# Performance work log

Hardware: AMD Instinct MI355X
Metric: run time of the kernel (lower is better)

The kernel has to match this reference:

```python
import jax, jax.numpy as jnp
import numpy as np

N, B, PG, L, HC, EC, H, NC, KNN = 256, 4, 64, 32, 128, 64, 4, 14, 8
D = HC // H
CUTOFF = 10.0
LOG2 = 0.6931471805599453

_counts = np.array([14, 5, 11, 8, 8, 6, 9, 9, 4, 10, 8, 8, 9, 8, 11, 7, 6, 7, 14, 12, 7])
RES_ATOM_MASK = (np.arange(14)[None, :] < _counts[:, None]).astype(np.float32)  # [21,14]


def _ln(x, g, b):
    mu = jnp.mean(x, -1, keepdims=True)
    var = jnp.mean((x - mu) ** 2, -1, keepdims=True)
    return (x - mu) / jnp.sqrt(var + 1e-5) * g + b


def _ssp(x):
    return jax.nn.softplus(x) - LOG2


def _safe_norm(x):
    return jnp.sqrt(jnp.maximum(jnp.sum(x * x, -1), 1e-12))


def _seg_softmax(x, idx, n):
    m = jax.ops.segment_max(x, idx, num_segments=n)
    e = jnp.exp(x - m[idx])
    s = jax.ops.segment_sum(e, idx, num_segments=n)
    return e / s[idx]


def _smear(d):
    offs = jnp.linspace(0.0, CUTOFF, EC)
    coeff = -0.5 / (offs[1] - offs[0]) ** 2
    return jnp.exp(coeff * (d[..., None] - offs) ** 2)


def _core(res_H, res_X, ligand_pos, ligand_feat, ligand_mask,
          ln_g, ln_b, ln1_g, ln1_b,
          WQ, WK, WV, WKl, WVl, WO, WOl, WOl1,
          Ti_w1, Ti_b1, Ti_w2, Ti_b2,
          sD_w1, sD_b1, sD_w2, sD_b2,
          sD1_w1, sD1_b1, sD1_w2, sD1_b2,
          res_S, batch, residue_mask, row1, col1):
    n = res_H.shape[0]
    bsz = ligand_feat.shape[0]
    lc = ligand_feat.shape[1]
    amask = jnp.asarray(RES_ATOM_MASK)[res_S]  # [n,14]

    # kNN graph on C-alpha (atom 1), per-graph, flow target_to_source, + self loops
    ctr = res_X[:, 1]
    d2 = jnp.sum((ctr[:, None] - ctr[None]) ** 2, -1)
    bad = (batch[:, None] != batch[None]) | jnp.eye(n, dtype=bool)
    _, nbr = jax.lax.top_k(-jnp.where(bad, jnp.inf, d2), KNN)
    row = jnp.concatenate([jnp.repeat(jnp.arange(n), KNN), jnp.arange(n)])
    col = jnp.concatenate([nbr.reshape(-1), jnp.arange(n)])

    Rij = _safe_norm(res_X[row][:, :, None] - res_X[col][:, None])  # [E,14,14]
    drep = _smear(Rij)  # [E,14,14,EC]

    res_Hn = _ln(res_H, ln_g, ln_b)
    Q = (res_Hn @ WQ.T).reshape(n, NC, H, D)
    Kt = (res_Hn @ WK.T).reshape(n, NC, H, D)
    V = (res_Hn @ WV.T).reshape(n, NC, H, D)

    logits = jnp.einsum('ephd,eqhd->ehpq', Q[row], Kt[col]) / np.sqrt(D)
    sig = jax.nn.relu(drep @ sD_w1.T + sD_b1) @ sD_w2.T + sD_b2  # [E,14,14,H]
    logits = logits + sig.transpose(0, 3, 1, 2)

    am_e = amask[row][:, :, None] * amask[col][:, None]  # [E,14,14]
    r = jnp.einsum('ep,ehpq,eq->eh', amask[row], logits, amask[col])
    r = r / jnp.sum(am_e, (-1, -2))[:, None]
    beta = _seg_softmax(r, row, n)  # [E,H]

    att = jax.nn.softmax(logits, -1) * am_e[:, None]
    att = att / (jnp.sum(jnp.abs(att), -1, keepdims=True) + 1e-7)
    aV = jnp.einsum('ehpq,eqhd->ehpd', att, V[col])
    updH = jax.ops.segment_sum(beta[:, :, None, None] * aV, row, num_segments=n)
    updH = updH.transpose(0, 2, 1, 3).reshape(n, NC, HC)
    res_H2 = (res_Hn + _ssp(updH) @ WO.T) * amask[..., None]

    Xij = res_X[row][:, :, None] - res_X[col][:, None]  # [E,14,14,3]
    Xij = Xij / (_safe_norm(Xij)[..., None] + 1e-5)
    Qf = Q.reshape(n, NC, HC)
    Kf = Kt.reshape(n, NC, HC)
    # T_i on concat([Q_p, K_q, dist]) computed as split matmuls (no big concat)
    hmid = (Qf[row] @ Ti_w1[:, :HC].T)[:, :, None, :] \
        + (Kf[col] @ Ti_w1[:, HC:2 * HC].T)[:, None, :, :] \
        + drep @ Ti_w1[:, 2 * HC:].T + Ti_b1  # [E,14,14,HC]
    f = (jax.nn.relu(hmid) @ Ti_w2.T + Ti_b2)[..., 0]  # [E,14,14]
    f = f * jnp.mean(att, 1)
    dX = jax.ops.segment_sum(jnp.mean(beta, -1)[:, None, None]
                             * jnp.sum(f[..., None] * Xij, -2), row, num_segments=n)
    res_X2 = jnp.where(residue_mask[:, None, None],
                       res_X + jnp.clip(dX, -3.0, 3.0), res_X)

    # residue <-> ligand cross attention over (editable residue, graph) edges
    lf = _ln(ligand_feat, ln1_g, ln1_b)
    Kl = (lf @ WKl.T).reshape(bsz, lc, H, D)
    Vl = (lf @ WVl.T).reshape(bsz, lc, H, D)
    Rij1 = _safe_norm(res_X2[row1][:, :, None] - ligand_pos[col1][:, None])
    drep1 = _smear(Rij1)  # [E1,14,L,EC]
    lg = jnp.einsum('ephd,eqhd->ehpq', Q[row1], Kl[col1]) / np.sqrt(D)
    sig1 = jax.nn.relu(drep1 @ sD1_w1.T + sD1_b1) @ sD1_w2.T + sD1_b2
    lg = lg + sig1.transpose(0, 3, 1, 2)

    am1 = amask[row1][:, :, None] * ligand_mask[col1][:, None]  # [E1,14,L]
    r1 = jnp.einsum('ep,ehpq,eq->eh', amask[row1], lg, ligand_mask[col1])
    r1 = r1 / jnp.sum(am1, (-1, -2))[:, None]
    beta1 = _seg_softmax(r1, col1, bsz)

    ar = jax.nn.softmax(lg, -1) * am1[:, None]
    ar = ar / (jnp.sum(jnp.abs(ar), -1, keepdims=True) + 1e-7)
    al = jax.nn.softmax(lg, -2) * am1[:, None]
    # faithful to source: lig branch divided by L1 norm of already-normalized ar
    al = al / (jnp.sum(jnp.abs(ar), -1, keepdims=True) + 1e-7)
    aVr = jnp.einsum('ehpq,eqhd->ehpd', ar, Vl[col1])  # [E1,H,14,D]
    e1 = row1.shape[0]
    res_H3 = res_H2.at[row1].add(
        _ssp(aVr.transpose(0, 2, 1, 3).reshape(e1, NC, HC)) @ WOl.T)
    res_H3 = res_H3 * amask[..., None]
    aVlg = jnp.einsum('ehpq,ephd->ehqd', al, V[row1])  # [E1,H,L,D]
    updL = jax.ops.segment_sum(beta1[:, :, None, None] * aVlg, col1, num_segments=bsz)
    lf2 = lf + _ssp(updL.transpose(0, 2, 1, 3).reshape(bsz, lc, HC)) @ WOl1.T
    return res_H3, res_X2, lf2


def setup_inputs() -> dict:
    key = jax.random.key(0)
    ks = jax.random.split(key, 40)
    rn = lambda i, shape, s=1.0: jax.random.normal(ks[i], shape, jnp.float32) * s
    w = lambda i, shape: jax.random.normal(ks[i], shape, jnp.float32) * 0.05
    res_H = rn(0, (N, NC, HC))
    res_X = rn(1, (N, NC, 3), 4.0)
    res_S = jax.random.randint(ks[2], (N,), 0, 21)
    batch = jnp.repeat(jnp.arange(B), PG)
    residue_mask = (jnp.arange(N) % PG) < 16
    row1 = jnp.asarray(np.nonzero(np.asarray(residue_mask))[0])
    col1 = row1 // PG
    ligand_pos = rn(3, (B, L, 3), 4.0)
    ligand_feat = rn(4, (B, L, HC))
    ligand_mask = jnp.tile((jnp.arange(L) < 24).astype(jnp.float32)[None], (B, 1))
    return dict(
        res_H=res_H, res_X=res_X, ligand_pos=ligand_pos, ligand_feat=ligand_feat,
        ligand_mask=ligand_mask,
        ln_g=jnp.ones((HC,)), ln_b=jnp.zeros((HC,)),
        ln1_g=jnp.ones((HC,)), ln1_b=jnp.zeros((HC,)),
        WQ=w(5, (HC, HC)), WK=w(6, (HC, HC)), WV=w(7, (HC, HC)),
        WKl=w(8, (HC, HC)), WVl=w(9, (HC, HC)),
        WO=w(10, (HC, HC)), WOl=w(11, (HC, HC)), WOl1=w(12, (HC, HC)),
        Ti_w1=w(13, (HC, 2 * HC + EC)), Ti_b1=jnp.zeros((HC,)),
        Ti_w2=w(14, (1, HC)), Ti_b2=jnp.zeros((1,)),
        sD_w1=w(15, (HC, EC)), sD_b1=jnp.zeros((HC,)),
        sD_w2=w(16, (H, HC)), sD_b2=jnp.zeros((H,)),
        sD1_w1=w(17, (HC, EC)), sD1_b1=jnp.zeros((HC,)),
        sD1_w2=w(18, (H, HC)), sD1_b2=jnp.zeros((H,)),
        res_S=res_S, batch=batch, residue_mask=residue_mask, row1=row1, col1=col1)


def reference(res_H, res_X, ligand_pos, ligand_feat, ligand_mask,
              ln_g, ln_b, ln1_g, ln1_b,
              WQ, WK, WV, WKl, WVl, WO, WOl, WOl1,
              Ti_w1, Ti_b1, Ti_w2, Ti_b2,
              sD_w1, sD_b1, sD_w2, sD_b2,
              sD1_w1, sD1_b1, sD1_w2, sD1_b2,
              res_S, batch, residue_mask, row1, col1):
    return _core(res_H, res_X, ligand_pos, ligand_feat, ligand_mask,
                 ln_g, ln_b, ln1_g, ln1_b,
                 WQ, WK, WV, WKl, WVl, WO, WOl, WOl1,
                 Ti_w1, Ti_b1, Ti_w2, Ti_b2,
                 sD_w1, sD_b1, sD_w2, sD_b2,
                 sD1_w1, sD1_b1, sD1_w2, sD1_b2,
                 res_S, batch, residue_mask, row1, col1)
```

## Files before the change

kernel.cpp:

```cpp
#include <hip/hip_runtime.h>
#include <hip/hip_bf16.h>
#include <math.h>

typedef __hip_bfloat16 bf16;

#define NRES 256
#define LC   32
#define HCH  128
#define ECH  64
#define NH   4
#define NCA  14
#define KNNK 8
#define DH   32
#define NKE  (NRES*KNNK)
#define NEDGE (NKE+NRES)
#define NE1  64
#define NROWS (NRES*NCA)

#define NT     3073
#define TSCALE 256.0f
#define DMAXT  12.0f

#define O_RESH   0
#define O_RESX   458752
#define O_LPOS   469504
#define O_LFEAT  469888
#define O_LMASK  486272
#define O_LNG    486400
#define O_LNB    486528
#define O_LN1G   486656
#define O_LN1B   486784
#define O_WQ     486912
#define O_WK     503296
#define O_WV     519680
#define O_WKL    536064
#define O_WVL    552448
#define O_WO     568832
#define O_WOL    585216
#define O_WOL1   601600
#define O_TIW1   617984
#define O_TIB1   658944
#define O_TIW2   659072
#define O_TIB2   659200
#define O_SDW1   659204
#define O_SDB1   667396
#define O_SDW2   667524
#define O_SDB2   668036
#define O_SD1W1  668040
#define O_SD1B1  676232
#define O_SD1W2  676360
#define O_SD1B2  676872
#define TOTCVT   676876
#define CVT_RSV  676880

#define OUTX_OFF 458752
#define OUTL_OFF 469504

__constant__ int c_counts[21] = {14,5,11,8,8,6,9,9,4,10,8,8,9,8,11,7,6,7,14,12,7};

__device__ __forceinline__ float b2f(bf16 x){ return __bfloat162float(x); }
__device__ __forceinline__ float sspf(float x){
  return fmaxf(x,0.f) + log1pf(expf(-fabsf(x))) - 0.6931471805599453f;
}
__device__ __forceinline__ float bflo(unsigned u){ return __uint_as_float(u<<16); }
__device__ __forceinline__ float bfhi(unsigned u){ return __uint_as_float(u & 0xffff0000u); }
__device__ __forceinline__ unsigned short f2bs(float v){ bf16 b=__float2bfloat16(v); return *(unsigned short*)&b; }
__device__ __forceinline__ unsigned pack2(float a, float b){
  return (unsigned)f2bs(a) | ((unsigned)f2bs(b)<<16);
}
__device__ __forceinline__ int ccount(int s){ return c_counts[s<0?0:(s>20?20:s)]; }
__device__ __forceinline__ void storeOut(void* out, int isbf, int idx, float v){
  if (isbf) ((bf16*)out)[idx] = __float2bfloat16(v);
  else      ((float*)out)[idx] = v;
}

__global__ __launch_bounds__(256) void kcvt(
    const void* s0,const void* s1,const void* s2,const void* s3,const void* s4,
    const void* s5,const void* s6,const void* s7,const void* s8,const void* s9,
    const void* s10,const void* s11,const void* s12,const void* s13,const void* s14,
    const void* s15,const void* s16,const void* s17,const void* s18,const void* s19,
    const void* s20,const void* s21,const void* s22,const void* s23,const void* s24,
    const void* s25,const void* s26,const void* s27,const void* s28,
    float* __restrict__ dst, int* __restrict__ flag)
{
  __shared__ int sflag;
  int tid = threadIdx.x;
  if (tid < 64){
    unsigned w = ((const unsigned*)s0)[tid];
    unsigned lo = w & 0xFFFFu;
    int ee = (lo >> 7) & 0xFF;
    int good = (lo == 0u) || (ee >= 121 && ee <= 133);
    unsigned long long m = __ballot(good);
    if (tid == 0){
      sflag = (__popcll(m) >= 40) ? 1 : 0;
      if (blockIdx.x == 0) flag[0] = sflag;
    }
  }
  __syncthreads();
  int isbf = sflag;
  int g = blockIdx.x*256 + tid;
  if (g >= TOTCVT) return;
  const void* src; int l;
  if      (g < O_RESX ) { src=s0;  l=g; }
  else if (g < O_LPOS ) { src=s1;  l=g-O_RESX; }
  else if (g < O_LFEAT) { src=s2;  l=g-O_LPOS; }
  else if (g < O_LMASK) { src=s3;  l=g-O_LFEAT; }
  else if (g < O_LNG  ) { src=s4;  l=g-O_LMASK; }
  else if (g < O_LNB  ) { src=s5;  l=g-O_LNG; }
  else if (g < O_LN1G ) { src=s6;  l=g-O_LNB; }
  else if (g < O_LN1B ) { src=s7;  l=g-O_LN1G; }
  else if (g < O_WQ   ) { src=s8;  l=g-O_LN1B; }
  else if (g < O_WK   ) { src=s9;  l=g-O_WQ; }
  else if (g < O_WV   ) { src=s10; l=g-O_WK; }
  else if (g < O_WKL  ) { src=s11; l=g-O_WV; }
  else if (g < O_WVL  ) { src=s12; l=g-O_WKL; }
  else if (g < O_WO   ) { src=s13; l=g-O_WVL; }
  else if (g < O_WOL  ) { src=s14; l=g-O_WO; }
  else if (g < O_WOL1 ) { src=s15; l=g-O_WOL; }
  else if (g < O_TIW1 ) { src=s16; l=g-O_WOL1; }
  else if (g < O_TIB1 ) { src=s17; l=g-O_TIW1; }
  else if (g < O_TIW2 ) { src=s18; l=g-O_TIB1; }
  else if (g < O_TIB2 ) { src=s19; l=g-O_TIW2; }
  else if (g < O_SDW1 ) { src=s20; l=0; }
  else if (g < O_SDB1 ) { src=s21; l=g-O_SDW1; }
  else if (g < O_SDW2 ) { src=s22; l=g-O_SDB1; }
  else if (g < O_SDB2 ) { src=s23; l=g-O_SDW2; }
  else if (g < O_SD1W1) { src=s24; l=g-O_SDB2; }
  else if (g < O_SD1B1) { src=s25; l=g-O_SD1W1; }
  else if (g < O_SD1W2) { src=s26; l=g-O_SD1B1; }
  else if (g < O_SD1B2) { src=s27; l=g-O_SD1W2; }
  else                  { src=s28; l=g-O_SD1B2; }
  float v = isbf ? b2f(((const bf16*)src)[l]) : ((const float*)src)[l];
  dst[g] = v;
}

__global__ __launch_bounds__(128) void kprep(const float* __restrict__ cvt, const int* __restrict__ row1,
    float* __restrict__ cT, float* __restrict__ sigT, float* __restrict__ sig1T,
    float* __restrict__ wt, int* __restrict__ inv_row)
{
  int b = blockIdx.x, o = threadIdx.x;
  if (b >= NT){
    int cb = b - NT;
    if (cb < 1280){
      int gid = cb*128 + o;
      int m = gid >> 14;
      int j = gid & 16383;
      int oo = j >> 7, c = j & 127;
      float v;
      switch(m){
        case 0: v = cvt[O_WQ  + j]; break;
        case 1: v = cvt[O_WK  + j]; break;
        case 2: v = cvt[O_WV  + j]; break;
        case 3: v = cvt[O_WO  + j]; break;
        case 4: v = cvt[O_WKL + j]; break;
        case 5: v = cvt[O_WVL + j]; break;
        case 6: v = cvt[O_WOL + j]; break;
        case 7: v = cvt[O_WOL1+ j]; break;
        case 8: v = cvt[O_TIW1 + oo*320 + c]; break;
        default:v = cvt[O_TIW1 + oo*320 + 128 + c]; break;
      }
      wt[m*16384 + c*128 + oo] = v;
    } else {
      for (int i=o;i<NRES;i+=128) inv_row[i] = -1;
      __syncthreads();
      if (o < NE1) inv_row[row1[o] & 255] = o;
    }
    return;
  }
  __shared__ float dr[64];
  __shared__ float W[128*65];
  __shared__ float h1[128], h1b[128];
  float d = (float)b * (1.0f/256.0f);
  const float step = 10.0f/63.0f;
  const float coef = -0.5f/(step*step);
  if (o < 64){ float t = d - step*(float)o; dr[o] = expf(coef*t*t); }
  for (int idx=o; idx<8192; idx+=128){ int oo=idx>>6, k=idx&63; W[oo*65+k] = cvt[O_TIW1 + oo*320 + 256 + k]; }
  __syncthreads();
  {
    float c = cvt[O_TIB1+o];
    for (int k=0;k<64;k++) c += dr[k]*W[o*65+k];
    cT[b*128+o] = c;
  }
  __syncthreads();
  for (int idx=o; idx<8192; idx+=128){ int oo=idx>>6, k=idx&63; W[oo*65+k] = cvt[O_SDW1 + idx]; }
  __syncthreads();
  {
    float a = cvt[O_SDB1+o];
    for (int k=0;k<64;k++) a += dr[k]*W[o*65+k];
    h1[o] = fmaxf(a,0.f);
  }
  __syncthreads();
  for (int idx=o; idx<8192; idx+=128){ int oo=idx>>6, k=idx&63; W[oo*65+k] = cvt[O_SD1W1 + idx]; }
  __syncthreads();
  {
    float a2 = cvt[O_SD1B1+o];
    for (int k=0;k<64;k++) a2 += dr[k]*W[o*65+k];
    h1b[o] = fmaxf(a2,0.f);
  }
  __syncthreads();
  if (o < 8){
    int h = o & 3;
    const float* hh = (o<4)? h1 : h1b;
    int wbase = (o<4)? O_SDW2 : O_SD1W2;
    int bbase = (o<4)? O_SDB2 : O_SD1B2;
    float s = cvt[bbase + h];
    for (int k=0;k<128;k++) s += hh[k]*cvt[wbase + h*128 + k];
    if (o<4) sigT[b*4+h] = s; else sig1T[b*4+h] = s;
  }
}

__global__ __launch_bounds__(256) void kProjAll(
    const float* __restrict__ cvt, const float* __restrict__ wt, const int* __restrict__ batch,
    float* __restrict__ resHn, bf16* __restrict__ Qw16, bf16* __restrict__ Kw16,
    bf16* __restrict__ Vw16, bf16* __restrict__ TQw16, bf16* __restrict__ TKw16,
    int* __restrict__ nbr, float* __restrict__ lf, bf16* __restrict__ Klw16, bf16* __restrict__ Vlw16)
{
  __shared__ float Xs[16*129];
  __shared__ float x2[2][HCH];
  __shared__ float sred2[2][2];
  int bb = blockIdx.x, tid = threadIdx.x;

  if (bb < 672){
    int m = bb / 224;
    int rt = (bb % 224) * 16;
    for (int i=tid; i<16*128; i+=256){
      int r=i>>7, c=i&127;
      Xs[r*129+c] = cvt[O_RESH + (rt+r)*HCH + c];
    }
    __syncthreads();
    {
      int wave = tid>>6, lane = tid&63;
      int r = wave*4 + (lane>>4);
      int cb = lane & 15;
      float s=0;
      #pragma unroll
      for (int j=0;j<8;j++) s += Xs[r*129 + cb + 16*j];
      #pragma unroll
      for (int off=1; off<16; off<<=1) s += __shfl_xor(s, off);
      float mu = s*(1.f/HCH);
      float q=0;
      #pragma unroll
      for (int j=0;j<8;j++){ float dv = Xs[r*129+cb+16*j]-mu; q += dv*dv; }
      #pragma unroll
      for (int off=1; off<16; off<<=1) q += __shfl_xor(q, off);
      float inv = rsqrtf(q*(1.f/HCH) + 1e-5f);
      #pragma unroll
      for (int j=0;j<8;j++){
        int c = cb + 16*j;
        float xh = (Xs[r*129+c]-mu)*inv*cvt[O_LNG+c] + cvt[O_LNB+c];
        Xs[r*129+c] = xh;
        if (m==0) resHn[(rt+r)*HCH+c] = xh;
      }
    }
    __syncthreads();
    int tc = (tid & 31) * 4;
    int tr = (tid >> 5) * 2;
    const float* W = wt + m*16384;
    float a00=0,a01=0,a02=0,a03=0, a10=0,a11=0,a12=0,a13=0;
    for (int c=0;c<HCH;c++){
      float4 w4 = *(const float4*)(W + c*128 + tc);
      float x0 = Xs[tr*129 + c];
      float x1 = Xs[(tr+1)*129 + c];
      a00 += x0*w4.x; a01 += x0*w4.y; a02 += x0*w4.z; a03 += x0*w4.w;
      a10 += x1*w4.x; a11 += x1*w4.y; a12 += x1*w4.z; a13 += x1*w4.w;
    }
    bf16* out = (m==0)? Qw16 : (m==1)? Kw16 : Vw16;
    {
      unsigned* o0 = (unsigned*)(out + (rt+tr  )*HCH + tc);
      unsigned* o1 = (unsigned*)(out + (rt+tr+1)*HCH + tc);
      o0[0]=pack2(a00,a01); o0[1]=pack2(a02,a03);
      o1[0]=pack2(a10,a11); o1[1]=pack2(a12,a13);
    }
    if (m == 2) return;
    __syncthreads();
    Xs[tr*129+tc]=a00; Xs[tr*129+tc+1]=a01; Xs[tr*129+tc+2]=a02; Xs[tr*129+tc+3]=a03;
    Xs[(tr+1)*129+tc]=a10; Xs[(tr+1)*129+tc+1]=a11; Xs[(tr+1)*129+tc+2]=a12; Xs[(tr+1)*129+tc+3]=a13;
    __syncthreads();
    const float* W2 = wt + (8+m)*16384;
    a00=0;a01=0;a02=0;a03=0; a10=0;a11=0;a12=0;a13=0;
    for (int c=0;c<HCH;c++){
      float4 w4 = *(const float4*)(W2 + c*128 + tc);
      float x0 = Xs[tr*129 + c];
      float x1 = Xs[(tr+1)*129 + c];
      a00 += x0*w4.x; a01 += x0*w4.y; a02 += x0*w4.z; a03 += x0*w4.w;
      a10 += x1*w4.x; a11 += x1*w4.y; a12 += x1*w4.z; a13 += x1*w4.w;
    }
    bf16* out2 = m ? TKw16 : TQw16;
    {
      unsigned* o0 = (unsigned*)(out2 + (rt+tr  )*HCH + tc);
      unsigned* o1 = (unsigned*)(out2 + (rt+tr+1)*HCH + tc);
      o0[0]=pack2(a00,a01); o0[1]=pack2(a02,a03);
      o1[0]=pack2(a10,a11); o1[1]=pack2(a12,a13);
    }
    return;
  }

  if (bb < 736){
    int wave = tid>>6, lane = tid&63;
    int n = (bb-672)*4 + wave;
    float cx = cvt[O_RESX+(n*NCA+1)*3+0];
    float cy = cvt[O_RESX+(n*NCA+1)*3+1];
    float cz = cvt[O_RESX+(n*NCA+1)*3+2];
    int bn = batch[n];
    float d2v[4]; int idv[4];
    #pragma unroll
    for (int t=0;t<4;t++){
      int j = lane + 64*t;
      float jx = cvt[O_RESX+(j*NCA+1)*3+0];
      float jy = cvt[O_RESX+(j*NCA+1)*3+1];
      float jz = cvt[O_RESX+(j*NCA+1)*3+2];
      float dx=cx-jx, dy=cy-jy, dz=cz-jz;
      float d2 = dx*dx+dy*dy+dz*dz;
      bool bad = (batch[j]!=bn) || (j==n);
      d2v[t] = bad ? INFINITY : d2;
      idv[t] = j;
    }
    for (int k=0;k<KNNK;k++){
      float dm = d2v[0]; int im = idv[0];
      #pragma unroll
      for (int t=1;t<4;t++)
        if (d2v[t]<dm || (d2v[t]==dm && idv[t]<im)){ dm=d2v[t]; im=idv[t]; }
      #pragma unroll
      for (int off=1; off<64; off<<=1){
        float dn = __shfl_xor(dm, off);
        int   in = __shfl_xor(im, off);
        if (dn<dm || (dn==dm && in<im)){ dm=dn; im=in; }
      }
      if (lane==0) nbr[n*KNNK+k] = im;
      #pragma unroll
      for (int t=0;t<4;t++) if (idv[t]==im) d2v[t] = INFINITY;
    }
    return;
  }

  int row = tid>>7, t = tid&127;
  int rb = (bb-736)*2 + row;
  float v = cvt[O_LFEAT + rb*HCH + t];
  float s=v;
  for (int off=1; off<64; off<<=1) s += __shfl_xor(s, off);
  if ((t&63)==0) sred2[row][t>>6]=s;
  __syncthreads();
  float mu=(sred2[row][0]+sred2[row][1])*(1.f/HCH);
  __syncthreads();
  float d=v-mu; s=d*d;
  for (int off=1; off<64; off<<=1) s += __shfl_xor(s, off);
  if ((t&63)==0) sred2[row][t>>6]=s;
  __syncthreads();
  float var=(sred2[row][0]+sred2[row][1])*(1.f/HCH);
  float xh = d*rsqrtf(var+1e-5f)*cvt[O_LN1G+t] + cvt[O_LN1B+t];
  x2[row][t]=xh; lf[rb*HCH+t]=xh;
  __syncthreads();
  const float* WKlt = wt + 4*16384;
  const float* WVlt = wt + 5*16384;
  float aK=0.f, aV=0.f;
  for (int c=0;c<HCH;c++){
    float xc=x2[row][c];
    aK += xc*WKlt[c*128+t];
    aV += xc*WVlt[c*128+t];
  }
  Klw16[rb*HCH+t]=__float2bfloat16(aK);
  Vlw16[rb*HCH+t]=__float2bfloat16(aV);
}

__global__ __launch_bounds__(256) void k3_edge(
    const float* __restrict__ cvt, const int* __restrict__ res_S, const int* __restrict__ nbr,
    const bf16* __restrict__ Qw16, const bf16* __restrict__ Kw16,
    const bf16* __restrict__ TQw16, const bf16* __restrict__ TKw16,
    const bf16* __restrict__ Vw16, const float* __restrict__ cT, const float* __restrict__ sigT,
    float* __restrict__ r_ws, bf16* __restrict__ aVe16, float* __restrict__ dXe)
{
  __shared__ unsigned Bq[14*66], Bk[14*66], Tq[14*66], Tk[14*66];
  __shared__ float LG[784], FR[196];
  __shared__ float tw2s[128], tb2s[1], Xr[42], Xc[42], amr[14], amc[14], rpart[56], cnts[2];
  unsigned* Vc = Tq;

  int b = blockIdx.x, tid = threadIdx.x;
  int rr = b & 255, slot = b >> 8;
  int e  = (slot < 8) ? (rr*8 + slot) : (2048 + rr);
  int cc = (slot < 8) ? (nbr[rr*8 + slot] & 255) : rr;

  const unsigned* Q32  = (const unsigned*)Qw16;
  const unsigned* K32  = (const unsigned*)Kw16;
  const unsigned* TQ32 = (const unsigned*)TQw16;
  const unsigned* TK32 = (const unsigned*)TKw16;
  const unsigned* V32  = (const unsigned*)Vw16;

  for (int i=tid;i<NCA*64;i+=256){
    int p=i>>6, k=i&63;
    Bq[p*66+k]=Q32[rr*896+i];  Bk[p*66+k]=K32[cc*896+i];
    Tq[p*66+k]=TQ32[rr*896+i]; Tk[p*66+k]=TK32[cc*896+i];
  }
  if (tid < 128) tw2s[tid]=cvt[O_TIW2+tid];
  if (tid == 128) tb2s[0]=cvt[O_TIB2];
  if (tid >= 136 && tid < 178){
    int i=tid-136; int p=i/3, jx=i%3;
    Xr[i] = cvt[O_RESX+(rr*NCA+p)*3+jx];
    Xc[i] = cvt[O_RESX+(cc*NCA+p)*3+jx];
  }
  if (tid >= 242 && tid < 242+NCA){
    int p=tid-242;
    amr[p] = (p < ccount(res_S[rr])) ? 1.f : 0.f;
    amc[p] = (p < ccount(res_S[cc])) ? 1.f : 0.f;
  }
  __syncthreads();

  if (tid < 196){
    int p = tid/14, q = tid%14;
    float dx=Xr[p*3]-Xc[q*3], dy=Xr[p*3+1]-Xc[q*3+1], dz=Xr[p*3+2]-Xc[q*3+2];
    float d = sqrtf(fmaxf(dx*dx+dy*dy+dz*dz, 1e-12f));
    int i0 = (int)(fminf(d, DMAXT)*TSCALE + 0.5f);
    float4 sg = ((const float4*)sigT)[i0];
    const float4* crow = (const float4*)(cT + i0*128);
    const uint2* Tq2 = (const uint2*)Tq;
    const uint2* Tk2 = (const uint2*)Tk;
    const uint2* Bq2 = (const uint2*)Bq;
    const uint2* Bk2 = (const uint2*)Bk;
    float fa = tb2s[0];
    #pragma unroll 8
    for (int j=0;j<32;j++){
      float4 cb = crow[j];
      uint2 ta = Tq2[p*33 + j];
      uint2 ka = Tk2[q*33 + j];
      int o = 4*j;
      fa += fmaxf(bflo(ta.x)+bflo(ka.x)+cb.x, 0.f)*tw2s[o  ];
      fa += fmaxf(bfhi(ta.x)+bfhi(ka.x)+cb.y, 0.f)*tw2s[o+1];
      fa += fmaxf(bflo(ta.y)+bflo(ka.y)+cb.z, 0.f)*tw2s[o+2];
      fa += fmaxf(bfhi(ta.y)+bfhi(ka.y)+cb.w, 0.f)*tw2s[o+3];
    }
    float qk0=0,qk1=0,qk2=0,qk3=0;
    #pragma unroll
    for (int j=0;j<8;j++){
      uint2 a0=Bq2[p*33+j],    b0=Bk2[q*33+j];
      uint2 a1=Bq2[p*33+8+j],  b1=Bk2[q*33+8+j];
      uint2 a2=Bq2[p*33+16+j], b2=Bk2[q*33+16+j];
      uint2 a3=Bq2[p*33+24+j], b3=Bk2[q*33+24+j];
      qk0 += bflo(a0.x)*bflo(b0.x) + bfhi(a0.x)*bfhi(b0.x) + bflo(a0.y)*bflo(b0.y) + bfhi(a0.y)*bfhi(b0.y);
      qk1 += bflo(a1.x)*bflo(b1.x) + bfhi(a1.x)*bfhi(b1.x) + bflo(a1.y)*bflo(b1.y) + bfhi(a1.y)*bfhi(b1.y);
      qk2 += bflo(a2.x)*bflo(b2.x) + bfhi(a2.x)*bfhi(b2.x) + bflo(a2.y)*bflo(b2.y) + bfhi(a2.y)*bfhi(b2.y);
      qk3 += bflo(a3.x)*bflo(b3.x) + bfhi(a3.x)*bfhi(b3.x) + bflo(a3.y)*bflo(b3.y) + bfhi(a3.y)*bfhi(b3.y);
    }
    const float isq = 0.17677669529663687f;
    LG[0*196+tid] = qk0*isq + sg.x;
    LG[1*196+tid] = qk1*isq + sg.y;
    LG[2*196+tid] = qk2*isq + sg.z;
    LG[3*196+tid] = qk3*isq + sg.w;
    FR[tid] = fa;
  }
  __syncthreads();

  for (int i=tid;i<NCA*64;i+=256){
    int p=i>>6, k=i&63;
    Vc[p*66+k]=V32[cc*896+i];
  }
  if (tid < 56){
    int h=tid/14, pp=tid%14;
    float ap = amr[pp];
    float row[NCA];
    float s=0;
    #pragma unroll
    for (int qq=0;qq<NCA;qq++){ row[qq]=LG[h*196+pp*14+qq]; s += row[qq]*amc[qq]; }
    rpart[h*14+pp] = s*ap;
    float m=-INFINITY;
    #pragma unroll
    for (int qq=0;qq<NCA;qq++) m=fmaxf(m,row[qq]);
    float sum=0;
    #pragma unroll
    for (int qq=0;qq<NCA;qq++){ row[qq]=expf(row[qq]-m); sum+=row[qq]; }
    float inv=1.f/sum, s2=0;
    #pragma unroll
    for (int qq=0;qq<NCA;qq++){ row[qq]=row[qq]*inv*ap*amc[qq]; s2+=row[qq]; }
    float inv2=1.f/(s2+1e-7f);
    #pragma unroll
    for (int qq=0;qq<NCA;qq++) LG[h*196+pp*14+qq]=row[qq]*inv2;
  }
  if (tid == 56){
    float sr=0, sc=0;
    for (int i=0;i<NCA;i++){ sr+=amr[i]; sc+=amc[i]; }
    cnts[0]=sr; cnts[1]=sc;
  }
  __syncthreads();
  if (tid < NH){
    float s=0;
    for (int pp=0;pp<NCA;pp++) s += rpart[tid*14+pp];
    r_ws[e*NH+tid] = s/(cnts[0]*cnts[1]);
  }
  if (tid < 196){
    int p=tid/14, q=tid%14;
    float ma = 0.25f*(LG[p*14+q] + LG[196+p*14+q] + LG[392+p*14+q] + LG[588+p*14+q]);
    FR[tid] *= ma;
  }
  __syncthreads();
  if (tid < NCA){
    int pp=tid;
    float ax=0, ay=0, az=0;
    #pragma unroll
    for (int qq=0;qq<NCA;qq++){
      float dx=Xr[pp*3]-Xc[qq*3], dy=Xr[pp*3+1]-Xc[qq*3+1], dz=Xr[pp*3+2]-Xc[qq*3+2];
      float nrm = sqrtf(fmaxf(dx*dx+dy*dy+dz*dz,1e-12f));
      float sc = FR[pp*14+qq]/(nrm+1e-5f);
      ax += sc*dx; ay += sc*dy; az += sc*dz;
    }
    dXe[(e*NCA+pp)*3+0]=ax; dXe[(e*NCA+pp)*3+1]=ay; dXe[(e*NCA+pp)*3+2]=az;
  }
  unsigned* aVe32 = (unsigned*)aVe16;
  #pragma unroll
  for (int rep=0;rep<4;rep++){
    int jdx = rep*256 + tid;
    if (jdx < 896){
      int h = jdx/224, rem = jdx%224;
      int pp = rem>>4, ddp = rem&15;
      float a0=0, a1=0;
      #pragma unroll
      for (int qq=0;qq<NCA;qq++){
        unsigned v = Vc[qq*66 + h*16 + ddp];
        float l = LG[h*196+pp*14+qq];
        a0 += l*bflo(v);
        a1 += l*bfhi(v);
      }
      aVe32[e*896 + jdx] = pack2(a0,a1);
    }
  }
}

__global__ __launch_bounds__(256) void k4_agg(
    const float* __restrict__ cvt, const int* __restrict__ res_S, const int* __restrict__ inv_row,
    const float* __restrict__ r_ws, const bf16* __restrict__ aVe16, const float* __restrict__ dXe,
    const float* __restrict__ resHn, const float* __restrict__ wt, const int* __restrict__ flag,
    float* __restrict__ resH2, float* __restrict__ resX2, void* __restrict__ d_out)
{
  int n = blockIdx.x, tid = threadIdx.x;
  __shared__ float beta[9][NH];
  __shared__ float betam[9];
  __shared__ float Xs[NCA][HCH];
  if (tid < NH){
    int h = tid;
    float rv[9], m=-INFINITY;
    #pragma unroll
    for (int k=0;k<9;k++){
      int ek = (k<KNNK)? n*KNNK+k : NKE+n;
      rv[k] = r_ws[ek*NH+h];
      m = fmaxf(m, rv[k]);
    }
    float s=0;
    #pragma unroll
    for (int k=0;k<9;k++){ rv[k]=expf(rv[k]-m); s+=rv[k]; }
    #pragma unroll
    for (int k=0;k<9;k++) beta[k][h]=rv[k]/s;
  }
  __syncthreads();
  if (tid < 9) betam[tid] = 0.25f*(beta[tid][0]+beta[tid][1]+beta[tid][2]+beta[tid][3]);
  int col = tid & 127, ph = tid >> 7;
  int h = col>>5, dd = col&31;
  float bh[9];
  #pragma unroll
  for (int k=0;k<9;k++) bh[k]=beta[k][h];
  #pragma unroll
  for (int i=0;i<7;i++){
    int p = ph + 2*i;
    float u=0;
    #pragma unroll
    for (int k=0;k<9;k++){
      int ek = (k<KNNK)? n*KNNK+k : NKE+n;
      u += bh[k]*b2f(aVe16[ek*1792 + h*448 + p*32 + dd]);
    }
    Xs[p][col] = sspf(u);
  }
  __syncthreads();
  const float* WOt = wt + 3*16384;
  float acc[7];
  #pragma unroll
  for (int i=0;i<7;i++) acc[i]=0.f;
  for (int c=0;c<HCH;c++){
    float w = WOt[c*128+col];
    #pragma unroll
    for (int i=0;i<7;i++) acc[i] += Xs[ph+2*i][c]*w;
  }
  int cnt = ccount(res_S[n]);
  #pragma unroll
  for (int i=0;i<7;i++){
    int p = ph + 2*i;
    float am = (p<cnt)?1.f:0.f;
    float outv = (resHn[(n*NCA+p)*HCH+col] + acc[i])*am;
    resH2[(n*NCA+p)*HCH+col] = outv;
  }
  if (tid < NCA*3){
    int isbf = *flag;
    int p=tid/3, jx=tid%3;
    float s=0;
    #pragma unroll
    for (int k=0;k<9;k++){
      int ek=(k<KNNK)? n*KNNK+k : NKE+n;
      s += betam[k]*dXe[(ek*NCA+p)*3+jx];
    }
    float base = cvt[O_RESX+(n*NCA+p)*3+jx];
    float v = (inv_row[n]>=0) ? base + fminf(fmaxf(s,-3.f),3.f) : base;
    resX2[(n*NCA+p)*3+jx] = v;
    storeOut(d_out, isbf, OUTX_OFF + (n*NCA+p)*3+jx, v);
  }
}

__global__ __launch_bounds__(256) void k6_lig(
    const float* __restrict__ cvt, const int* __restrict__ res_S,
    const int* __restrict__ row1, const int* __restrict__ col1,
    const float* __restrict__ resX2, const bf16* __restrict__ Qw16, const bf16* __restrict__ Klw16,
    const bf16* __restrict__ Vw16, const bf16* __restrict__ Vlw16, const float* __restrict__ sig1T,
    float* __restrict__ r1_ws, float* __restrict__ aVr, float* __restrict__ aVlg)
{
  __shared__ __align__(16) float S[10042];
  float* Bq  = S;
  float* Bk  = S + 1848;
  float* LG  = S;
  float* Vl  = S + 1848;
  float* ALs = S + 6104;
  float* Vr  = S + 7896;
  float* EX  = S + 9744;
  float* Xr = EX;
  float* Lp = EX + 42;
  float* amr = EX + 138;
  float* lm  = EX + 152;
  float* s2r = EX + 184;
  float* rpart = EX + 240;
  float* cnts  = EX + 296;
  int e = blockIdx.x, tid = threadIdx.x;
  int rr = row1[e] & 255, cb = col1[e] & 3;

  for (int i=tid;i<NCA*HCH;i+=256){ int p=i>>7,c=i&127; Bq[p*132+c]=b2f(Qw16[rr*1792+i]); Vr[p*132+c]=b2f(Vw16[rr*1792+i]); }
  for (int i=tid;i<LC*HCH;i+=256){ int q=i>>7,c=i&127; Bk[q*133+c]=b2f(Klw16[cb*LC*HCH+i]); }
  if (tid >= 8 && tid < 50){ int i=tid-8; int p=i/3,jx=i%3; Xr[i]=resX2[(rr*NCA+p)*3+jx]; }
  if (tid >= 64 && tid < 160){ int i=tid-64; int q=i/3,jx=i%3; Lp[i]=cvt[O_LPOS+(cb*LC+q)*3+jx]; }
  if (tid >= 160 && tid < 160+NCA) amr[tid-160]=((tid-160) < ccount(res_S[rr]))?1.f:0.f;
  if (tid >= 192 && tid < 224) lm[tid-192]=cvt[O_LMASK + cb*LC + tid-192];
  __syncthreads();

  float l0[2][4];
  int npair = (tid < 192) ? 2 : 1;
  for (int w=0; w<npair; w++){
    int pair = tid + w*256;
    int p = pair>>5, q = pair&31;
    float dx=Xr[p*3]-Lp[q*3], dy=Xr[p*3+1]-Lp[q*3+1], dz=Xr[p*3+2]-Lp[q*3+2];
    float d = sqrtf(fmaxf(dx*dx+dy*dy+dz*dz,1e-12f));
    int i0 = (int)(fminf(d, DMAXT)*TSCALE + 0.5f);
    float4 sg = ((const float4*)sig1T)[i0];
    float q0=0,q1=0,q2=0,q3=0;
    #pragma unroll
    for (int dd=0;dd<DH;dd++){
      q0 += Bq[p*132+dd]   *Bk[q*133+dd];
      q1 += Bq[p*132+32+dd]*Bk[q*133+32+dd];
      q2 += Bq[p*132+64+dd]*Bk[q*133+64+dd];
      q3 += Bq[p*132+96+dd]*Bk[q*133+96+dd];
    }
    const float isq=0.17677669529663687f;
    l0[w][0]=q0*isq+sg.x; l0[w][1]=q1*isq+sg.y; l0[w][2]=q2*isq+sg.z; l0[w][3]=q3*isq+sg.w;
  }
  __syncthreads();
  for (int w=0; w<npair; w++){
    int pair = tid + w*256;
    LG[0*448+pair]=l0[w][0]; LG[1*448+pair]=l0[w][1]; LG[2*448+pair]=l0[w][2]; LG[3*448+pair]=l0[w][3];
  }
  for (int i=tid;i<LC*HCH;i+=256){ int q=i>>7,c=i&127; Vl[q*132+c]=b2f(Vlw16[cb*LC*HCH+i]); }
  __syncthreads();

  if (tid < 56){
    int h=tid/14, pp=tid%14;
    float ap=amr[pp];
    float s=0, m=-INFINITY;
    for (int qq=0;qq<LC;qq++){ float v=LG[h*448+pp*32+qq]; s+=v*lm[qq]; m=fmaxf(m,v); }
    rpart[h*14+pp]=s*ap;
    float sum=0;
    for (int qq=0;qq<LC;qq++) sum+=expf(LG[h*448+pp*32+qq]-m);
    float inv=1.f/sum, s2=0;
    for (int qq=0;qq<LC;qq++) s2 += expf(LG[h*448+pp*32+qq]-m)*inv*ap*lm[qq];
    s2r[h*14+pp] = s2/(s2+1e-7f);
  }
  if (tid==56){
    float sr=0,sl=0;
    for(int i=0;i<NCA;i++) sr+=amr[i];
    for(int i=0;i<LC;i++) sl+=lm[i];
    cnts[0]=sr; cnts[1]=sl;
  }
  __syncthreads();
  if (tid < NH){
    float s=0; for (int pp=0;pp<NCA;pp++) s+=rpart[tid*14+pp];
    r1_ws[e*NH+tid]=s/(cnts[0]*cnts[1]);
  }
  if (tid < NH*LC){
    int h=tid>>5, qq=tid&31;
    float m=-INFINITY;
    for (int pp=0;pp<NCA;pp++) m=fmaxf(m,LG[h*448+pp*32+qq]);
    float sum=0;
    for (int pp=0;pp<NCA;pp++) sum+=expf(LG[h*448+pp*32+qq]-m);
    float inv=1.f/sum;
    float lq=lm[qq];
    for (int pp=0;pp<NCA;pp++){
      float a=expf(LG[h*448+pp*32+qq]-m)*inv*amr[pp]*lq;
      ALs[h*448+pp*32+qq]=a/(s2r[h*14+pp]+1e-7f);
    }
  }
  __syncthreads();
  if (tid < 56){
    int h=tid/14, pp=tid%14;
    float ap=amr[pp];
    float m=-INFINITY;
    for (int qq=0;qq<LC;qq++) m=fmaxf(m,LG[h*448+pp*32+qq]);
    float row[LC];
    float sum=0;
    for (int qq=0;qq<LC;qq++){ row[qq]=expf(LG[h*448+pp*32+qq]-m); sum+=row[qq]; }
    float inv=1.f/sum, s2=0;
    for (int qq=0;qq<LC;qq++){ row[qq]=row[qq]*inv*ap*lm[qq]; s2+=row[qq]; }
    float inv2=1.f/(s2+1e-7f);
    for (int qq=0;qq<LC;qq++) LG[h*448+pp*32+qq]=row[qq]*inv2;
  }
  __syncthreads();
  for (int j=tid;j<NH*NCA*DH;j+=256){
    int h=j/448, rem=j%448, pp=rem>>5, dd=rem&31;
    float acc=0;
    #pragma unroll
    for (int qq=0;qq<LC;qq++) acc += LG[h*448+pp*32+qq]*Vl[qq*132+h*32+dd];
    aVr[e*1792+j]=acc;
  }
  for (int j=tid;j<NH*LC*DH;j+=256){
    int h=j>>10, rem=j&1023, qq=rem>>5, dd=rem&31;
    float acc=0;
    #pragma unroll
    for (int pp=0;pp<NCA;pp++) acc += ALs[h*448+pp*32+qq]*Vr[pp*132+h*32+dd];
    aVlg[e*4096+j]=acc;
  }
}

__global__ __launch_bounds__(256) void k78_final(
    const int* __restrict__ inv_row, const int* __restrict__ res_S, const int* __restrict__ col1,
    const float* __restrict__ resH2, const float* __restrict__ aVr,
    const float* __restrict__ r1_ws, const float* __restrict__ aVlg, const float* __restrict__ lf,
    const float* __restrict__ wt, const int* __restrict__ flag, void* __restrict__ d_out)
{
  int bb = blockIdx.x, tid = threadIdx.x;
  if (bb < 256){
    int n = bb;
    int e = inv_row[n];
    __shared__ float G[NCA][HCH];
    if (e>=0){
      for (int j=tid;j<NCA*HCH;j+=256){
        int h=j/448, rem=j%448, pp=rem>>5, dd=rem&31;
        G[pp][h*DH+dd] = sspf(aVr[e*1792+j]);
      }
    }
    __syncthreads();
    int col = tid & 127, ph = tid >> 7;
    float acc[7];
    #pragma unroll
    for (int i=0;i<7;i++) acc[i]=0.f;
    if (e>=0){
      const float* WOlt = wt + 6*16384;
      for (int c=0;c<HCH;c++){
        float w=WOlt[c*128+col];
        #pragma unroll
        for (int i=0;i<7;i++) acc[i]+=G[ph+2*i][c]*w;
      }
    }
    int cnt=ccount(res_S[n]);
    int isbf = *flag;
    #pragma unroll
    for (int i=0;i<7;i++){
      int p = ph + 2*i;
      float am=(p<cnt)?1.f:0.f;
      float v=(resH2[(n*NCA+p)*HCH+col]+acc[i])*am;
      storeOut(d_out, isbf, (n*NCA+p)*HCH+col, v);
    }
    return;
  }
  int rb = bb - 256;
  int b = rb>>5, q = rb&31;
  __shared__ float bw[NE1][NH];
  __shared__ float xs[HCH];
  if (tid<NH){
    int h=tid;
    float m=-INFINITY;
    for (int e=0;e<NE1;e++) if ((col1[e]&3)==b) m=fmaxf(m, r1_ws[e*NH+h]);
    float s=0;
    for (int e=0;e<NE1;e++) if ((col1[e]&3)==b) s+=expf(r1_ws[e*NH+h]-m);
    for (int e=0;e<NE1;e++) bw[e][h] = ((col1[e]&3)==b)? expf(r1_ws[e*NH+h]-m)/s : 0.f;
  }
  __syncthreads();
  if (tid < 128){
    int h=tid>>5, dd=tid&31;
    float u=0;
    for (int e=0;e<NE1;e++) u += bw[e][h]*aVlg[e*4096 + h*1024 + q*32 + dd];
    xs[tid]=sspf(u);
  }
  __syncthreads();
  if (tid < 128){
    const float* WOl1t = wt + 7*16384;
    float acc=0;
    for (int c=0;c<HCH;c++) acc += xs[c]*WOl1t[c*128+tid];
    float v = lf[rb*HCH+tid] + acc;
    storeOut(d_out, *flag, OUTL_OFF + rb*HCH+tid, v);
  }
}

extern "C" void kernel_launch(void* const* d_in, const int* in_sizes, int n_in,
                              void* d_out, int out_size, void* d_ws, size_t ws_size,
                              hipStream_t stream)
{
  const int* res_S = (const int*)d_in[29];
  const int* batch = (const int*)d_in[30];
  const int* row1  = (const int*)d_in[32];
  const int* col1  = (const int*)d_in[33];

  float* wsf = (float*)d_ws;
  size_t o = 0;
  int*   flag    = (int*)(wsf + o); o += 4;
  float* cvt     = wsf + o; o += CVT_RSV;
  float* wt      = wsf + o; o += 10*16384;
  int*   inv_row = (int*)(wsf + o); o += 256;
  int*   nbr     = (int*)(wsf + o); o += NRES*KNNK;
  float* resHn   = wsf + o; o += NROWS*HCH;
  bf16*  Qw16    = (bf16*)(wsf + o); o += NROWS*HCH/2;
  bf16*  Kw16    = (bf16*)(wsf + o); o += NROWS*HCH/2;
  bf16*  Vw16    = (bf16*)(wsf + o); o += NROWS*HCH/2;
  bf16*  TQw16   = (bf16*)(wsf + o); o += NROWS*HCH/2;
  bf16*  TKw16   = (bf16*)(wsf + o); o += NROWS*HCH/2;
  float* r_ws    = wsf + o; o += NEDGE*NH;
  bf16*  aVe16   = (bf16*)(wsf + o); o += (size_t)NEDGE*1792/2;
  float* dXe     = wsf + o; o += NEDGE*NCA*3;
  float* resH2   = wsf + o; o += NROWS*HCH;
  float* resX2   = wsf + o; o += NRES*NCA*3;
  float* lf      = wsf + o; o += 4*LC*HCH;
  bf16*  Klw16   = (bf16*)(wsf + o); o += 4*LC*HCH/2;
  bf16*  Vlw16   = (bf16*)(wsf + o); o += 4*LC*HCH/2;
  float* r1w     = wsf + o; o += NE1*NH;
  float* aVrw    = wsf + o; o += NE1*1792;
  float* aVlgw   = wsf + o; o += NE1*4096;
  float* cT      = wsf + o; o += (size_t)NT*128;
  float* sigT    = wsf + o; o += NT*4;
  float* sig1T   = wsf + o; o += NT*4;

  kcvt<<<(TOTCVT+255)/256, 256, 0, stream>>>(
      d_in[0],d_in[1],d_in[2],d_in[3],d_in[4],d_in[5],d_in[6],d_in[7],d_in[8],
      d_in[9],d_in[10],d_in[11],d_in[12],d_in[13],d_in[14],d_in[15],d_in[16],
      d_in[17],d_in[18],d_in[19],d_in[20],d_in[21],d_in[22],d_in[23],d_in[24],
      d_in[25],d_in[26],d_in[27],d_in[28], cvt, flag);
  kprep<<<NT + 1280 + 1, 128, 0, stream>>>(cvt, row1, cT, sigT, sig1T, wt, inv_row);
  kProjAll<<<800, 256, 0, stream>>>(cvt, wt, batch, resHn, Qw16, Kw16, Vw16, TQw16, TKw16,
                                    nbr, lf, Klw16, Vlw16);
  k3_edge<<<NEDGE, 256, 0, stream>>>(cvt, res_S, nbr, Qw16, Kw16, TQw16, TKw16, Vw16, cT, sigT,
                                     r_ws, aVe16, dXe);
  k4_agg<<<NRES, 256, 0, stream>>>(cvt, res_S, inv_row, r_ws, aVe16, dXe, resHn, wt, flag,
                                   resH2, resX2, d_out);
  k6_lig<<<NE1, 256, 0, stream>>>(cvt, res_S, row1, col1, resX2, Qw16, Klw16, Vw16, Vlw16, sig1T,
                                  r1w, aVrw, aVlgw);
  k78_final<<<384, 256, 0, stream>>>(inv_row, res_S, col1, resH2, aVrw, r1w, aVlgw, lf,
                                     wt, flag, d_out);
}
```

Measured before the change: 282.6 us.

## Use MFMA bf16 instructions for per-edge QK logits and attention-V products

Replaces the scalar bf16 dot products for the 14x14 per-head QK logits and the attention-weighted V aggregation in the edge kernel with 16x16x32 bf16 MFMA instructions, using XOR-swizzled shared-memory layouts for Q, K and a transposed V. The pairwise trigger-MLP inputs are pre-expanded to fp32 in shared memory so the inner loop no longer unpacks bf16. The aim is to cut ALU work in the edge kernel. In exchange it pads 14 to 16, rounds attention weights to bf16 before the V product, adds an extra barrier, and writes aVe as scattered 2-byte stores.

Result: no change. 285.3 us (+1.0%).

```diff
diff --git a/kernel.cpp b/kernel.cpp
--- a/kernel.cpp
+++ b/kernel.cpp
@@ -57,6 +57,9 @@
 #define OUTL_OFF 469504
 
 __constant__ int c_counts[21] = {14,5,11,8,8,6,9,9,4,10,8,8,9,8,11,7,6,7,14,12,7};
+
+using bfrag = __attribute__((ext_vector_type(8))) short;
+using f32x4 = __attribute__((ext_vector_type(4))) float;
 
 __device__ __forceinline__ float b2f(bf16 x){ return __bfloat162float(x); }
 __device__ __forceinline__ float sspf(float x){
@@ -369,26 +372,53 @@
     const bf16* __restrict__ Vw16, const float* __restrict__ cT, const float* __restrict__ sigT,
     float* __restrict__ r_ws, bf16* __restrict__ aVe16, float* __restrict__ dXe)
 {
-  __shared__ unsigned Bq[14*66], Bk[14*66], Tq[14*66], Tk[14*66];
-  __shared__ float LG[784], FR[196];
+  __shared__ __align__(16) unsigned char QbB[16*256];
+  __shared__ __align__(16) unsigned char KbB[16*256];
+  __shared__ __align__(16) unsigned char VtB[128*64];
+  __shared__ __align__(16) float Tq32[14*132];
+  __shared__ __align__(16) float Tk32[14*132];
+  __shared__ __align__(16) float LG[4*16*20];
+  __shared__ float FR[196];
   __shared__ float tw2s[128], tb2s[1], Xr[42], Xc[42], amr[14], amc[14], rpart[56], cnts[2];
-  unsigned* Vc = Tq;
 
   int b = blockIdx.x, tid = threadIdx.x;
   int rr = b & 255, slot = b >> 8;
   int e  = (slot < 8) ? (rr*8 + slot) : (2048 + rr);
   int cc = (slot < 8) ? (nbr[rr*8 + slot] & 255) : rr;
 
-  const unsigned* Q32  = (const unsigned*)Qw16;
-  const unsigned* K32  = (const unsigned*)Kw16;
-  const unsigned* TQ32 = (const unsigned*)TQw16;
-  const unsigned* TK32 = (const unsigned*)TKw16;
-  const unsigned* V32  = (const unsigned*)Vw16;
-
-  for (int i=tid;i<NCA*64;i+=256){
-    int p=i>>6, k=i&63;
-    Bq[p*66+k]=Q32[rr*896+i];  Bk[p*66+k]=K32[cc*896+i];
-    Tq[p*66+k]=TQ32[rr*896+i]; Tk[p*66+k]=TK32[cc*896+i];
+  {
+    int row = tid >> 4, s16 = tid & 15;
+    uint4 qv = {0u,0u,0u,0u}, kv = {0u,0u,0u,0u};
+    if (row < 14){
+      qv = ((const uint4*)(Qw16 + (size_t)rr*1792))[tid];
+      kv = ((const uint4*)(Kw16 + (size_t)cc*1792))[tid];
+    }
+    int off = row*256 + ((s16 ^ (row & 7)) << 4);
+    *(uint4*)(QbB + off) = qv;
+    *(uint4*)(KbB + off) = kv;
+  }
+  for (int i = tid; i < 14*64; i += 256){
+    int p = i >> 6, k2 = i & 63;
+    unsigned tq = ((const unsigned*)(TQw16 + (size_t)rr*1792))[i];
+    unsigned tk = ((const unsigned*)(TKw16 + (size_t)cc*1792))[i];
+    Tq32[p*132 + 2*k2  ] = bflo(tq);
+    Tq32[p*132 + 2*k2+1] = bfhi(tq);
+    Tk32[p*132 + 2*k2  ] = bflo(tk);
+    Tk32[p*132 + 2*k2+1] = bfhi(tk);
+  }
+  for (int i = tid; i < 128*16; i += 256){
+    int qp = i >> 7, d = i & 127;
+    int qq = qp*2;
+    unsigned pv = 0u;
+    if (qq < 14){
+      const unsigned short* vs = (const unsigned short*)(Vw16 + (size_t)cc*1792);
+      unsigned short v0 = vs[qq*128 + d];
+      unsigned short v1 = vs[(qq+1)*128 + d];
+      pv = (unsigned)v0 | ((unsigned)v1 << 16);
+    }
+    int slotq = qq >> 3;
+    int off = d*64 + ((slotq ^ (d & 3)) << 4) + (qq & 7)*2;
+    *(unsigned*)(VtB + off) = pv;
   }
   if (tid < 128) tw2s[tid]=cvt[O_TIW2+tid];
   if (tid == 128) tb2s[0]=cvt[O_TIB2];
@@ -404,61 +434,67 @@
   }
   __syncthreads();
 
-  if (tid < 196){
+  {
+    int w = tid >> 6, l = tid & 63;
+    int mrow = l & 15, s = l >> 4;
+    int aoff = mrow*256 + (((w*4 + s) ^ (mrow & 7)) << 4);
+    bfrag a = *(const bfrag*)(QbB + aoff);
+    bfrag bkf = *(const bfrag*)(KbB + aoff);
+    f32x4 dacc = {0.f,0.f,0.f,0.f};
+    dacc = __builtin_amdgcn_mfma_f32_16x16x32_bf16(a, bkf, dacc, 0, 0, 0);
+    const float isq = 0.17677669529663687f;
+    #pragma unroll
+    for (int r=0;r<4;r++){
+      int p = s*4 + r;
+      LG[w*320 + p*20 + mrow] = dacc[r]*isq;
+    }
+  }
+
+  float sgx=0.f, sgy=0.f, sgz=0.f, sgw=0.f;
+  int havePair = (tid < 196);
+  if (havePair){
     int p = tid/14, q = tid%14;
     float dx=Xr[p*3]-Xc[q*3], dy=Xr[p*3+1]-Xc[q*3+1], dz=Xr[p*3+2]-Xc[q*3+2];
     float d = sqrtf(fmaxf(dx*dx+dy*dy+dz*dz, 1e-12f));
     int i0 = (int)(fminf(d, DMAXT)*TSCALE + 0.5f);
     float4 sg = ((const float4*)sigT)[i0];
+    sgx=sg.x; sgy=sg.y; sgz=sg.z; sgw=sg.w;
     const float4* crow = (const float4*)(cT + i0*128);
-    const uint2* Tq2 = (const uint2*)Tq;
-    const uint2* Tk2 = (const uint2*)Tk;
-    const uint2* Bq2 = (const uint2*)Bq;
-    const uint2* Bk2 = (const uint2*)Bk;
+    const float4* tqr = (const float4*)(Tq32 + p*132);
+    const float4* tkr = (const float4*)(Tk32 + q*132);
     float fa = tb2s[0];
     #pragma unroll 8
     for (int j=0;j<32;j++){
       float4 cb = crow[j];
-      uint2 ta = Tq2[p*33 + j];
-      uint2 ka = Tk2[q*33 + j];
+      float4 ta = tqr[j];
+      float4 ka = tkr[j];
       int o = 4*j;
-      fa += fmaxf(bflo(ta.x)+bflo(ka.x)+cb.x, 0.f)*tw2s[o  ];
-      fa += fmaxf(bfhi(ta.x)+bfhi(ka.x)+cb.y, 0.f)*tw2s[o+1];
-      fa += fmaxf(bflo(ta.y)+bflo(ka.y)+cb.z, 0.f)*tw2s[o+2];
-      fa += fmaxf(bfhi(ta.y)+bfhi(ka.y)+cb.w, 0.f)*tw2s[o+3];
-    }
-    float qk0=0,qk1=0,qk2=0,qk3=0;
-    #pragma unroll
-    for (int j=0;j<8;j++){
-      uint2 a0=Bq2[p*33+j],    b0=Bk2[q*33+j];
-      uint2 a1=Bq2[p*33+8+j],  b1=Bk2[q*33+8+j];
-      uint2 a2=Bq2[p*33+16+j], b2=Bk2[q*33+16+j];
-      uint2 a3=Bq2[p*33+24+j], b3=Bk2[q*33+24+j];
-      qk0 += bflo(a0.x)*bflo(b0.x) + bfhi(a0.x)*bfhi(b0.x) + bflo(a0.y)*bflo(b0.y) + bfhi(a0.y)*bfhi(b0.y);
-      qk1 += bflo(a1.x)*bflo(b1.x) + bfhi(a1.x)*bfhi(b1.x) + bflo(a1.y)*bflo(b1.y) + bfhi(a1.y)*bfhi(b1.y);
-      qk2 += bflo(a2.x)*bflo(b2.x) + bfhi(a2.x)*bfhi(b2.x) + bflo(a2.y)*bflo(b2.y) + bfhi(a2.y)*bfhi(b2.y);
-      qk3 += bflo(a3.x)*bflo(b3.x) + bfhi(a3.x)*bfhi(b3.x) + bflo(a3.y)*bflo(b3.y) + bfhi(a3.y)*bfhi(b3.y);
-    }
-    const float isq = 0.17677669529663687f;
-    LG[0*196+tid] = qk0*isq + sg.x;
-    LG[1*196+tid] = qk1*isq + sg.y;
-    LG[2*196+tid] = qk2*isq + sg.z;
-    LG[3*196+tid] = qk3*isq + sg.w;
+      fa += fmaxf(ta.x+ka.x+cb.x, 0.f)*tw2s[o  ];
+      fa += fmaxf(ta.y+ka.y+cb.y, 0.f)*tw2s[o+1];
+      fa += fmaxf(ta.z+ka.z+cb.z, 0.f)*tw2s[o+2];
+      fa += fmaxf(ta.w+ka.w+cb.w, 0.f)*tw2s[o+3];
+    }
     FR[tid] = fa;
   }
   __syncthreads();
 
-  for (int i=tid;i<NCA*64;i+=256){
-    int p=i>>6, k=i&63;
-    Vc[p*66+k]=V32[cc*896+i];
-  }
+  if (havePair){
+    int p = tid/14, q = tid%14;
+    LG[      p*20+q] += sgx;
+    LG[320 + p*20+q] += sgy;
+    LG[640 + p*20+q] += sgz;
+    LG[960 + p*20+q] += sgw;
+  }
+  __syncthreads();
+
   if (tid < 56){
     int h=tid/14, pp=tid%14;
     float ap = amr[pp];
+    float* rowp = LG + h*320 + pp*20;
     float row[NCA];
     float s=0;
     #pragma unroll
-    for (int qq=0;qq<NCA;qq++){ row[qq]=LG[h*196+pp*14+qq]; s += row[qq]*amc[qq]; }
+    for (int qq=0;qq<NCA;qq++){ row[qq]=rowp[qq]; s += row[qq]*amc[qq]; }
     rpart[h*14+pp] = s*ap;
     float m=-INFINITY;
     #pragma unroll
@@ -471,7 +507,7 @@
     for (int qq=0;qq<NCA;qq++){ row[qq]=row[qq]*inv*ap*amc[qq]; s2+=row[qq]; }
     float inv2=1.f/(s2+1e-7f);
     #pragma unroll
-    for (int qq=0;qq<NCA;qq++) LG[h*196+pp*14+qq]=row[qq]*inv2;
+    for (int qq=0;qq<NCA;qq++) rowp[qq]=row[qq]*inv2;
   }
   if (tid == 56){
     float sr=0, sc=0;
@@ -486,10 +522,11 @@
   }
   if (tid < 196){
     int p=tid/14, q=tid%14;
-    float ma = 0.25f*(LG[p*14+q] + LG[196+p*14+q] + LG[392+p*14+q] + LG[588+p*14+q]);
+    float ma = 0.25f*(LG[p*20+q] + LG[320+p*20+q] + LG[640+p*20+q] + LG[960+p*20+q]);
     FR[tid] *= ma;
   }
   __syncthreads();
+
   if (tid < NCA){
     int pp=tid;
     float ax=0, ay=0, az=0;
@@ -502,22 +539,32 @@
     }
     dXe[(e*NCA+pp)*3+0]=ax; dXe[(e*NCA+pp)*3+1]=ay; dXe[(e*NCA+pp)*3+2]=az;
   }
-  unsigned* aVe32 = (unsigned*)aVe16;
-  #pragma unroll
-  for (int rep=0;rep<4;rep++){
-    int jdx = rep*256 + tid;
-    if (jdx < 896){
-      int h = jdx/224, rem = jdx%224;
-      int pp = rem>>4, ddp = rem&15;
-      float a0=0, a1=0;
-      #pragma unroll
-      for (int qq=0;qq<NCA;qq++){
-        unsigned v = Vc[qq*66 + h*16 + ddp];
-        float l = LG[h*196+pp*14+qq];
-        a0 += l*bflo(v);
-        a1 += l*bfhi(v);
+
+  {
+    int w = tid >> 6, l = tid & 63;
+    int mrow = l & 15, s = l >> 4;
+    bfrag pa;
+    if (s < 2){
+      const float* ar = LG + w*320 + mrow*20 + s*8;
+      #pragma unroll
+      for (int j=0;j<8;j++) pa[j] = (short)f2bs(ar[j]);
+    } else {
+      #pragma unroll
+      for (int j=0;j<8;j++) pa[j] = (short)0;
+    }
+    #pragma unroll
+    for (int half=0; half<2; half++){
+      int dg = w*32 + half*16 + mrow;
+      int boff = dg*64 + ((s ^ (dg & 3)) << 4);
+      bfrag pb = *(const bfrag*)(VtB + boff);
+      f32x4 dd = {0.f,0.f,0.f,0.f};
+      dd = __builtin_amdgcn_mfma_f32_16x16x32_bf16(pa, pb, dd, 0, 0, 0);
+      #pragma unroll
+      for (int r=0;r<4;r++){
+        int p = s*4 + r;
+        if (p < NCA)
+          aVe16[(size_t)e*1792 + w*448 + p*32 + half*16 + mrow] = __float2bfloat16(dd[r]);
       }
-      aVe32[e*896 + jdx] = pack2(a0,a1);
     }
   }
 }
```
